# Performance work log

Measured on AMD Instinct MI355X. Metric: run time of the kernel, lower is better.

The kernel has to match this reference:

```python
import jax, jax.numpy as jnp
import numpy as np

T, N, F_IN, H1, H2, F_OUT = 48, 4096, 64, 64, 32, 64

def setup_inputs() -> dict:
    key = jax.random.key(0)
    ks = jax.random.split(key, 14)
    sc = 0.05
    x = jax.random.normal(ks[0], (T, N, F_IN), jnp.float32)
    adj = jax.random.uniform(ks[1], (N, N), jnp.float32) / N  # roughly row-normalized dense adjacency
    fc_w = jax.random.normal(ks[2], (F_IN, H1), jnp.float32) * sc
    fc_b = jnp.zeros((H1,), jnp.float32)
    Wz = jax.random.normal(ks[3], (H1, F_OUT), jnp.float32) * sc
    Wr = jax.random.normal(ks[4], (H1, F_OUT), jnp.float32) * sc
    Wh = jax.random.normal(ks[5], (H1, F_OUT), jnp.float32) * sc
    Lz = jax.random.normal(ks[6], (2 * F_OUT, F_OUT), jnp.float32) * sc
    Lr = jax.random.normal(ks[7], (2 * F_OUT, F_OUT), jnp.float32) * sc
    Lh = jax.random.normal(ks[8], (2 * F_OUT, F_OUT), jnp.float32) * sc
    bz = jnp.zeros((F_OUT,), jnp.float32)
    br = jnp.zeros((F_OUT,), jnp.float32)
    bh = jnp.zeros((F_OUT,), jnp.float32)
    return {"x": x, "adj": adj, "fc_w": fc_w, "fc_b": fc_b,
            "Wz": Wz, "Wr": Wr, "Wh": Wh,
            "Lz": Lz, "Lr": Lr, "Lh": Lh,
            "bz": bz, "br": br, "bh": bh}

def reference(x, adj, fc_w, fc_b, Wz, Wr, Wh, Lz, Lr, Lh, bz, br, bh):
    # relu(fc(x)) followed by relu(unsqueeze) == single relu
    xh = jax.nn.relu(x @ fc_w + fc_b)          # [T, N, H1]
    h0 = jnp.zeros((N, F_OUT), x.dtype)

    def step(h, xi):
        # TGCN cell: dense graph conv A @ (X W) feeding GRU-style gates
        az = adj @ (xi @ Wz)                   # [N, F_OUT]
        ar = adj @ (xi @ Wr)
        ah = adj @ (xi @ Wh)
        z = jax.nn.sigmoid(jnp.concatenate([az, h], axis=-1) @ Lz + bz)
        r = jax.nn.sigmoid(jnp.concatenate([ar, h], axis=-1) @ Lr + br)
        h_tilde = jnp.tanh(jnp.concatenate([ah, h * r], axis=-1) @ Lh + bh)
        h_new = z * h + (1.0 - z) * h_tilde
        return h_new, None

    h, _ = jax.lax.scan(step, h0, xh)
    return h[None]                              # [1, N, F_OUT]
```

## Files before the change

### kernel.cpp

```cpp
#include <hip/hip_runtime.h>

typedef unsigned short u16;
typedef unsigned char u8;
typedef short s16x8 __attribute__((ext_vector_type(8)));
typedef unsigned short u16x4 __attribute__((ext_vector_type(4)));
typedef float f32x4 __attribute__((ext_vector_type(4)));
typedef int i32x4 __attribute__((ext_vector_type(4)));
typedef int i32x8 __attribute__((ext_vector_type(8)));

#define AS1 __attribute__((address_space(1)))
#define AS3 __attribute__((address_space(3)))

__device__ __forceinline__ void g2l16(const void* g, void* l) {
  __builtin_amdgcn_global_load_lds((const AS1 void*)g, (AS3 void*)l, 16, 0, 0);
}

__device__ __forceinline__ float b2f(u16 u) {
  union { unsigned int i; float f; } x; x.i = ((unsigned int)u) << 16; return x.f;
}
__device__ __forceinline__ u16 f2b(float f) {
  unsigned int u = __builtin_bit_cast(unsigned int, f);
  return (u16)((u + 0x7fffu + ((u >> 16) & 1u)) >> 16);
}
__device__ __forceinline__ u8 f2e4m3(float v) {
  int p = __builtin_amdgcn_cvt_pk_fp8_f32(v, 0.f, 0, false);
  return (u8)(p & 0xff);
}
__device__ __forceinline__ float sigm(float x) { return 1.f / (1.f + __expf(-x)); }
__device__ __forceinline__ float tanh_f(float x) { return 2.f / (1.f + __expf(-2.f * x)) - 1.f; }


__global__ __launch_bounds__(256) void kpre(
    const float* __restrict__ a, u8* __restrict__ ab,
    const float* __restrict__ fcw, const float* __restrict__ fcb,
    const float* __restrict__ x, u8* __restrict__ xht,
    const float* __restrict__ Wz, const float* __restrict__ Wr, const float* __restrict__ Wh,
    const float* __restrict__ Lz, const float* __restrict__ Lr, const float* __restrict__ Lh,
    u16* __restrict__ wct, u16* __restrict__ lbt) {
  int b = blockIdx.x, tid = threadIdx.x;
  if (b < 4096) {
    size_t idx = (size_t)b * 256 + tid;
    const float4* src = (const float4*)a;
    unsigned int* dst = (unsigned int*)ab;
#pragma unroll
    for (int k = 0; k < 4; ++k) {
      float4 v = src[idx + (size_t)k * 1048576];
      unsigned int p = __builtin_amdgcn_cvt_pk_fp8_f32(v.x * 4096.f, v.y * 4096.f, 0, false);
      p = __builtin_amdgcn_cvt_pk_fp8_f32(v.z * 4096.f, v.w * 4096.f, p, true);
      dst[idx + (size_t)k * 1048576] = p;
    }
    return;
  }
  if (b < 4144) {
    int idx = (b - 4096) * 256 + tid;
    int c_cat = idx >> 6, hh = idx & 63;
    int g = c_cat >> 6, c = c_cat & 63;
    const float* W = (g == 0) ? Wz : (g == 1) ? Wr : Wh;
    const float* L = (g == 0) ? Lz : (g == 1) ? Lr : Lh;
    float acc = 0.f;
    for (int m = 0; m < 64; ++m) acc += W[hh * 64 + m] * L[m * 64 + c];
    wct[c_cat * 64 + hh] = f2b(acc);
    return;
  }
  if (b < 4147) {
    int g = b - 4144;
    const float* L = (g == 0) ? Lz : (g == 1) ? Lr : Lh;
    for (int i = 0; i < 16; ++i) {
      int idx = tid * 16 + i; int c = idx >> 6, hh = idx & 63;
      lbt[g * 4096 + c * 64 + hh] = f2b(L[(64 + hh) * 64 + c]);
    }
    return;
  }
  int kb = b - 4147;
  int t = kb >> 5, n0 = (kb & 31) * 128;
  __shared__ __align__(16) u16 xs[128 * 72];
  __shared__ __align__(16) u16 fw[64 * 72];
  __shared__ __align__(16) u8 xh8[64 * 128];
  __shared__ float fb[64];
  int w = tid >> 6, l = tid & 63;
#pragma unroll
  for (int i = 0; i < 16; ++i) {
    int idx = tid + i * 256;
    int h = idx & 63, f = idx >> 6;
    fw[h * 72 + f] = f2b(fcw[f * 64 + h]);
  }
  const float4* xg = (const float4*)(x + ((size_t)t * 4096 + n0) * 64);
#pragma unroll
  for (int i = 0; i < 8; ++i) {
    int f = tid + i * 256;
    float4 v = xg[f];
    u16x4 p; p[0] = f2b(v.x); p[1] = f2b(v.y); p[2] = f2b(v.z); p[3] = f2b(v.w);
    *(u16x4*)&xs[(f >> 4) * 72 + (f & 15) * 4] = p;
  }
  if (tid < 64) fb[tid] = fcb[tid];
  __syncthreads();

  int lm = l & 15, q = l >> 4;
  f32x4 acc[4][2];
#pragma unroll
  for (int i = 0; i < 4; ++i)
#pragma unroll
    for (int j = 0; j < 2; ++j)
#pragma unroll
      for (int r = 0; r < 4; ++r) acc[i][j][r] = 0.f;
#pragma unroll
  for (int s = 0; s < 2; ++s) {
    s16x8 af[4], bf[2];
#pragma unroll
    for (int i = 0; i < 4; ++i) af[i] = *(const s16x8*)&fw[(16 * i + lm) * 72 + 32 * s + q * 8];
#pragma unroll
    for (int j = 0; j < 2; ++j) bf[j] = *(const s16x8*)&xs[(32 * w + 16 * j + lm) * 72 + 32 * s + q * 8];
#pragma unroll
    for (int i = 0; i < 4; ++i)
#pragma unroll
      for (int j = 0; j < 2; ++j)
        acc[i][j] = __builtin_amdgcn_mfma_f32_16x16x32_bf16(af[i], bf[j], acc[i][j], 0, 0, 0);
  }
#pragma unroll
  for (int i = 0; i < 4; ++i)
#pragma unroll
    for (int j = 0; j < 2; ++j) {
      int node = 32 * w + 16 * j + lm;
      int h0 = 16 * i + q * 4;
#pragma unroll
      for (int r = 0; r < 4; ++r) {
        float v = acc[i][j][r] + fb[h0 + r];
        xh8[(h0 + r) * 128 + node] = f2e4m3(v > 0.f ? v : 0.f);
      }
    }
  __syncthreads();
  {
    int h = tid >> 2, seg = tid & 3;
    u8* dst = xht + (size_t)(t * 64 + h) * 4096 + n0 + seg * 32;
    const u8* src = &xh8[h * 128 + seg * 32];
    *(i32x4*)dst = *(const i32x4*)src;
    *(i32x4*)(dst + 16) = *(const i32x4*)(src + 16);
  }
}

__global__ __launch_bounds__(256) void k2(
    const u8* __restrict__ A, const u8* __restrict__ B, u16* __restrict__ M) {
  __shared__ __align__(16) u8 sh[81920];
  int tid = threadIdx.x, w = tid >> 6, l = tid & 63;
  int nt = blockIdx.x, mt = blockIdx.y;
  const u8* Ab = A + (size_t)mt * 128 * 4096;
  const u8* Bb = B + (size_t)nt * 192 * 4096;
  int lm = l & 15, q = l >> 4;
  int wm = w >> 1, wn = w & 1;
  int srow = l >> 3, scol = l & 7;
  f32x4 acc[4][6];
#pragma unroll
  for (int i = 0; i < 4; ++i)
#pragma unroll
    for (int j = 0; j < 6; ++j)
#pragma unroll
      for (int r = 0; r < 4; ++r) acc[i][j][r] = 0.f;

#define STAGE(bsel, kk)                                                       \
  do {                                                                        \
    u8* As_ = sh + (bsel) * 40960;                                            \
    u8* Bs_ = As_ + 16384;                                                    \
    _Pragma("unroll") for (int j = 0; j < 4; ++j) {      \
      int r0 = 32 * w + 8 * j;                                                \
      int row = r0 + srow;                                                    \
      int c = (scol - row) & 7;                                               \
      g2l16(Ab + (size_t)row * 4096 + (kk) + c * 16, As_ + r0 * 128);         \
    }                                                                         \
    _Pragma("unroll") for (int j = 0; j < 6; ++j) {      \
      int r0 = 48 * w + 8 * j;                                                \
      int row = r0 + srow;                                                    \
      int c = (scol - row) & 7;                                               \
      g2l16(Bb + (size_t)row * 4096 + (kk) + c * 16, Bs_ + r0 * 128);         \
    }                                                                         \
  } while (0)

  STAGE(0, 0);
  __syncthreads();

  for (int it = 0; it < 32; ++it) {
    int k0b = it * 128;
    int cur = it & 1;
    if (it < 31) STAGE(cur ^ 1, k0b + 128);
    const u8* As = sh + cur * 40960;
    const u8* Bs = As + 16384;
    i32x8 a8[4];
#pragma unroll
    for (int i = 0; i < 4; ++i) {
      int ra = 64 * wm + 16 * i + lm;
      int p0 = (2 * q + ra) & 7, p1 = (2 * q + 1 + ra) & 7;
      i32x4 lo = *(const i32x4*)&As[ra * 128 + p0 * 16];
      i32x4 hi = *(const i32x4*)&As[ra * 128 + p1 * 16];
      a8[i] = __builtin_shufflevector(lo, hi, 0, 1, 2, 3, 4, 5, 6, 7);
    }
#pragma unroll
    for (int j = 0; j < 6; ++j) {
      int rb = 96 * wn + 16 * j + lm;
      int q0 = (2 * q + rb) & 7, q1 = (2 * q + 1 + rb) & 7;
      i32x4 lo2 = *(const i32x4*)&Bs[rb * 128 + q0 * 16];
      i32x4 hi2 = *(const i32x4*)&Bs[rb * 128 + q1 * 16];
      i32x8 b8 = __builtin_shufflevector(lo2, hi2, 0, 1, 2, 3, 4, 5, 6, 7);
#pragma unroll
      for (int i = 0; i < 4; ++i)
        acc[i][j] = __builtin_amdgcn_mfma_scale_f32_16x16x128_f8f6f4(
            a8[i], b8, acc[i][j], 0, 0, 0, 127, 0, 127);
    }
    __syncthreads();
  }
#undef STAGE

  u16* tb = (u16*)sh;
  const float sc = 1.f / 4096.f;
#pragma unroll
  for (int p = 0; p < 2; ++p) {
    if (p) __syncthreads();
    if (wm == p) {
#pragma unroll
      for (int i = 0; i < 4; ++i)
#pragma unroll
        for (int j = 0; j < 6; ++j)
#pragma unroll
          for (int r = 0; r < 4; ++r)
            tb[(16 * i + 4 * q + r) * 200 + 96 * wn + 16 * j + lm] = f2b(acc[i][j][r] * sc);
    }
    __syncthreads();
    int row = tid >> 2, seg = tid & 3;
    u16* dst = M + (size_t)(mt * 128 + p * 64 + row) * 3072 + nt * 192 + seg * 48;
    const u16* src = &tb[row * 200 + seg * 48];
#pragma unroll
    for (int v = 0; v < 6; ++v)
      *(i32x4*)(dst + 8 * v) = *(const i32x4*)(src + 8 * v);
  }
}

__global__ __launch_bounds__(256) void k3(
    const u16* __restrict__ M, const u16* __restrict__ wct, const u16* __restrict__ lbt,
    const float* __restrict__ bz, const float* __restrict__ br, const float* __restrict__ bh,
    float* __restrict__ out) {
  __shared__ __align__(16) u16 hhi[16 * 72], hlo[16 * 72];
  __shared__ __align__(16) u16 rhi[16 * 72], rlo[16 * 72];
  int tid = threadIdx.x, w = tid >> 6, l = tid & 63;
  int nb0 = blockIdx.x * 16;
  int lm = l & 15, q = l >> 4;
  int cb = 16 * w + q * 4;
  s16x8 afw[3][2], afl[3][2];
#pragma unroll
  for (int g = 0; g < 3; ++g)
#pragma unroll
    for (int s = 0; s < 2; ++s) {
      afw[g][s] = *(const s16x8*)&wct[(size_t)(g * 64 + 16 * w + lm) * 64 + 32 * s + q * 8];
      afl[g][s] = *(const s16x8*)&lbt[(size_t)(g * 64 + 16 * w + lm) * 64 + 32 * s + q * 8];
    }
  for (int i = tid; i < 16 * 72; i += 256) { hhi[i] = 0; hlo[i] = 0; }
  f32x4 bzv, brv, bhv, hv;
#pragma unroll
  for (int r = 0; r < 4; ++r) {
    bzv[r] = bz[cb + r]; brv[r] = br[cb + r]; bhv[r] = bh[cb + r]; hv[r] = 0.f;
  }
  __syncthreads();

  const u16* Mrow = M + (size_t)(nb0 + lm) * 3072;
  s16x8 Mn[2];
  Mn[0] = *(const s16x8*)&Mrow[q * 8];
  Mn[1] = *(const s16x8*)&Mrow[32 + q * 8];

  for (int t = 0; t < 48; ++t) {
    s16x8 Mc[2] = {Mn[0], Mn[1]};
    if (t < 47) {
      Mn[0] = *(const s16x8*)&Mrow[(t + 1) * 64 + q * 8];
      Mn[1] = *(const s16x8*)&Mrow[(t + 1) * 64 + 32 + q * 8];
    }
    f32x4 uzw, uzh, urw, urh;
#pragma unroll
    for (int r = 0; r < 4; ++r) { uzw[r] = 0.f; uzh[r] = 0.f; urw[r] = 0.f; urh[r] = 0.f; }
#pragma unroll
    for (int s = 0; s < 2; ++s) {
      s16x8 hh = *(const s16x8*)&hhi[lm * 72 + 32 * s + q * 8];
      s16x8 hl = *(const s16x8*)&hlo[lm * 72 + 32 * s + q * 8];
      uzw = __builtin_amdgcn_mfma_f32_16x16x32_bf16(afw[0][s], Mc[s], uzw, 0, 0, 0);
      uzh = __builtin_amdgcn_mfma_f32_16x16x32_bf16(afl[0][s], hh, uzh, 0, 0, 0);
      uzh = __builtin_amdgcn_mfma_f32_16x16x32_bf16(afl[0][s], hl, uzh, 0, 0, 0);
      urw = __builtin_amdgcn_mfma_f32_16x16x32_bf16(afw[1][s], Mc[s], urw, 0, 0, 0);
      urh = __builtin_amdgcn_mfma_f32_16x16x32_bf16(afl[1][s], hh, urh, 0, 0, 0);
      urh = __builtin_amdgcn_mfma_f32_16x16x32_bf16(afl[1][s], hl, urh, 0, 0, 0);
    }
    f32x4 zv, rv;
#pragma unroll
    for (int r = 0; r < 4; ++r) {
      zv[r] = sigm(uzw[r] + uzh[r] + bzv[r]);
      rv[r] = sigm(urw[r] + urh[r] + brv[r]);
    }
    {
      u16x4 phi, plo;
#pragma unroll
      for (int r = 0; r < 4; ++r) {
        float p = hv[r] * rv[r];
        u16 hi = f2b(p); phi[r] = hi; plo[r] = f2b(p - b2f(hi));
      }
      *(u16x4*)&rhi[lm * 72 + cb] = phi;
      *(u16x4*)&rlo[lm * 72 + cb] = plo;
    }
    __syncthreads();
    f32x4 uhw, uhh;
#pragma unroll
    for (int r = 0; r < 4; ++r) { uhw[r] = 0.f; uhh[r] = 0.f; }
#pragma unroll
    for (int s = 0; s < 2; ++s) {
      s16x8 rh = *(const s16x8*)&rhi[lm * 72 + 32 * s + q * 8];
      s16x8 rl = *(const s16x8*)&rlo[lm * 72 + 32 * s + q * 8];
      uhw = __builtin_amdgcn_mfma_f32_16x16x32_bf16(afw[2][s], Mc[s], uhw, 0, 0, 0);
      uhh = __builtin_amdgcn_mfma_f32_16x16x32_bf16(afl[2][s], rh, uhh, 0, 0, 0);
      uhh = __builtin_amdgcn_mfma_f32_16x16x32_bf16(afl[2][s], rl, uhh, 0, 0, 0);
    }
    {
      u16x4 phi, plo;
#pragma unroll
      for (int r = 0; r < 4; ++r) {
        float th = tanh_f(uhw[r] + uhh[r] + bhv[r]);
        float hn = zv[r] * hv[r] + (1.f - zv[r]) * th;
        hv[r] = hn;
        u16 hi = f2b(hn); phi[r] = hi; plo[r] = f2b(hn - b2f(hi));
      }
      *(u16x4*)&hhi[lm * 72 + cb] = phi;
      *(u16x4*)&hlo[lm * 72 + cb] = plo;
    }
    __syncthreads();
  }
#pragma unroll
  for (int r = 0; r < 4; ++r)
    out[(size_t)(nb0 + lm) * 64 + cb + r] = hv[r];
}

extern "C" void kernel_launch(void* const* d_in, const int* in_sizes, int n_in,
                              void* d_out, int out_size, void* d_ws, size_t ws_size,
                              hipStream_t stream) {
  const float* x   = (const float*)d_in[0];
  const float* adj = (const float*)d_in[1];
  const float* fcw = (const float*)d_in[2];
  const float* fcb = (const float*)d_in[3];
  const float* Wz  = (const float*)d_in[4];
  const float* Wr  = (const float*)d_in[5];
  const float* Wh  = (const float*)d_in[6];
  const float* Lz  = (const float*)d_in[7];
  const float* Lr  = (const float*)d_in[8];
  const float* Lh  = (const float*)d_in[9];
  const float* bz  = (const float*)d_in[10];
  const float* br  = (const float*)d_in[11];
  const float* bh  = (const float*)d_in[12];
  char* ws = (char*)d_ws;
  u8*  xht  = (u8*)(ws);
  u8*  adj8 = (u8*)(ws + (size_t)12582912);
  u16* Mm   = (u16*)(ws + (size_t)29360128);
  u16* wct  = (u16*)(ws + (size_t)54525952);
  u16* lbt  = (u16*)(ws + (size_t)54550528);
  float* outp = (float*)d_out;

  hipLaunchKernelGGL(kpre, dim3(5683), dim3(256), 0, stream,
                     adj, adj8, fcw, fcb, x, xht, Wz, Wr, Wh, Lz, Lr, Lh, wct, lbt);
  hipLaunchKernelGGL(k2, dim3(16, 32), dim3(256), 0, stream, adj8, xht, Mm);
  hipLaunchKernelGGL(k3, dim3(256), dim3(256), 0, stream, Mm, wct, lbt, bz, br, bh, outp);
}
```

Measured before the change: 259.3 us.

## Precompute next-step input MFMAs off the critical path and swizzle LDS hidden state

In the recurrent GRU kernel, the input-side MFMAs (M times gate weights, seeded with the bias) for step t+1 are now issued before the end-of-step barrier, so only the hidden-state MFMAs remain on the serial dependency chain. The hi and lo hidden-state products are split into independent accumulators to shorten MFMA dependency chains. The LDS layout changes from padded 72-element rows to 64-element rows with an XOR swizzle, meant to avoid bank conflicts while using less shared memory. It adds live registers for the precomputed accumulators.

```diff
diff --git a/kernel.cpp b/kernel.cpp
--- a/kernel.cpp
+++ b/kernel.cpp
@@ -236,12 +236,16 @@
     const u16* __restrict__ M, const u16* __restrict__ wct, const u16* __restrict__ lbt,
     const float* __restrict__ bz, const float* __restrict__ br, const float* __restrict__ bh,
     float* __restrict__ out) {
-  __shared__ __align__(16) u16 hhi[16 * 72], hlo[16 * 72];
-  __shared__ __align__(16) u16 rhi[16 * 72], rlo[16 * 72];
+  __shared__ __align__(16) u16 hhi[1024], hlo[1024];
+  __shared__ __align__(16) u16 rhi[1024], rlo[1024];
   int tid = threadIdx.x, w = tid >> 6, l = tid & 63;
   int nb0 = blockIdx.x * 16;
   int lm = l & 15, q = l >> 4;
+  int am = lm & 7;
   int cb = 16 * w + q * 4;
+  int rd0 = lm * 64 + ((q ^ am) * 8);
+  int rd1 = lm * 64 + (((4 + q) ^ am) * 8);
+  int wi  = lm * 64 + (((2 * w + (q >> 1)) ^ am) * 8) + 4 * (q & 1);
   s16x8 afw[3][2], afl[3][2];
 #pragma unroll
   for (int g = 0; g < 3; ++g)
@@ -250,44 +254,46 @@
       afw[g][s] = *(const s16x8*)&wct[(size_t)(g * 64 + 16 * w + lm) * 64 + 32 * s + q * 8];
       afl[g][s] = *(const s16x8*)&lbt[(size_t)(g * 64 + 16 * w + lm) * 64 + 32 * s + q * 8];
     }
-  for (int i = tid; i < 16 * 72; i += 256) { hhi[i] = 0; hlo[i] = 0; }
+  for (int i = tid; i < 1024; i += 256) { hhi[i] = 0; hlo[i] = 0; }
   f32x4 bzv, brv, bhv, hv;
 #pragma unroll
   for (int r = 0; r < 4; ++r) {
     bzv[r] = bz[cb + r]; brv[r] = br[cb + r]; bhv[r] = bh[cb + r]; hv[r] = 0.f;
   }
+  const f32x4 zf = {0.f, 0.f, 0.f, 0.f};
   __syncthreads();
 
   const u16* Mrow = M + (size_t)(nb0 + lm) * 3072;
   s16x8 Mn[2];
   Mn[0] = *(const s16x8*)&Mrow[q * 8];
   Mn[1] = *(const s16x8*)&Mrow[32 + q * 8];
+  f32x4 uzwC = __builtin_amdgcn_mfma_f32_16x16x32_bf16(afw[0][0], Mn[0], bzv, 0, 0, 0);
+  uzwC = __builtin_amdgcn_mfma_f32_16x16x32_bf16(afw[0][1], Mn[1], uzwC, 0, 0, 0);
+  f32x4 urwC = __builtin_amdgcn_mfma_f32_16x16x32_bf16(afw[1][0], Mn[0], brv, 0, 0, 0);
+  urwC = __builtin_amdgcn_mfma_f32_16x16x32_bf16(afw[1][1], Mn[1], urwC, 0, 0, 0);
+  f32x4 uhwC = __builtin_amdgcn_mfma_f32_16x16x32_bf16(afw[2][0], Mn[0], bhv, 0, 0, 0);
+  uhwC = __builtin_amdgcn_mfma_f32_16x16x32_bf16(afw[2][1], Mn[1], uhwC, 0, 0, 0);
 
   for (int t = 0; t < 48; ++t) {
-    s16x8 Mc[2] = {Mn[0], Mn[1]};
     if (t < 47) {
       Mn[0] = *(const s16x8*)&Mrow[(t + 1) * 64 + q * 8];
       Mn[1] = *(const s16x8*)&Mrow[(t + 1) * 64 + 32 + q * 8];
     }
-    f32x4 uzw, uzh, urw, urh;
-#pragma unroll
-    for (int r = 0; r < 4; ++r) { uzw[r] = 0.f; uzh[r] = 0.f; urw[r] = 0.f; urh[r] = 0.f; }
-#pragma unroll
-    for (int s = 0; s < 2; ++s) {
-      s16x8 hh = *(const s16x8*)&hhi[lm * 72 + 32 * s + q * 8];
-      s16x8 hl = *(const s16x8*)&hlo[lm * 72 + 32 * s + q * 8];
-      uzw = __builtin_amdgcn_mfma_f32_16x16x32_bf16(afw[0][s], Mc[s], uzw, 0, 0, 0);
-      uzh = __builtin_amdgcn_mfma_f32_16x16x32_bf16(afl[0][s], hh, uzh, 0, 0, 0);
-      uzh = __builtin_amdgcn_mfma_f32_16x16x32_bf16(afl[0][s], hl, uzh, 0, 0, 0);
-      urw = __builtin_amdgcn_mfma_f32_16x16x32_bf16(afw[1][s], Mc[s], urw, 0, 0, 0);
-      urh = __builtin_amdgcn_mfma_f32_16x16x32_bf16(afl[1][s], hh, urh, 0, 0, 0);
-      urh = __builtin_amdgcn_mfma_f32_16x16x32_bf16(afl[1][s], hl, urh, 0, 0, 0);
-    }
+    s16x8 hh0 = *(const s16x8*)&hhi[rd0], hh1 = *(const s16x8*)&hhi[rd1];
+    s16x8 hl0 = *(const s16x8*)&hlo[rd0], hl1 = *(const s16x8*)&hlo[rd1];
+    f32x4 uzA = __builtin_amdgcn_mfma_f32_16x16x32_bf16(afl[0][0], hh0, uzwC, 0, 0, 0);
+    uzA = __builtin_amdgcn_mfma_f32_16x16x32_bf16(afl[0][1], hh1, uzA, 0, 0, 0);
+    f32x4 uzB = __builtin_amdgcn_mfma_f32_16x16x32_bf16(afl[0][0], hl0, zf, 0, 0, 0);
+    uzB = __builtin_amdgcn_mfma_f32_16x16x32_bf16(afl[0][1], hl1, uzB, 0, 0, 0);
+    f32x4 urA = __builtin_amdgcn_mfma_f32_16x16x32_bf16(afl[1][0], hh0, urwC, 0, 0, 0);
+    urA = __builtin_amdgcn_mfma_f32_16x16x32_bf16(afl[1][1], hh1, urA, 0, 0, 0);
+    f32x4 urB = __builtin_amdgcn_mfma_f32_16x16x32_bf16(afl[1][0], hl0, zf, 0, 0, 0);
+    urB = __builtin_amdgcn_mfma_f32_16x16x32_bf16(afl[1][1], hl1, urB, 0, 0, 0);
     f32x4 zv, rv;
 #pragma unroll
     for (int r = 0; r < 4; ++r) {
-      zv[r] = sigm(uzw[r] + uzh[r] + bzv[r]);
-      rv[r] = sigm(urw[r] + urh[r] + brv[r]);
+      zv[r] = sigm(uzA[r] + uzB[r]);
+      rv[r] = sigm(urA[r] + urB[r]);
     }
     {
       u16x4 phi, plo;
@@ -296,32 +302,35 @@
         float p = hv[r] * rv[r];
         u16 hi = f2b(p); phi[r] = hi; plo[r] = f2b(p - b2f(hi));
       }
-      *(u16x4*)&rhi[lm * 72 + cb] = phi;
-      *(u16x4*)&rlo[lm * 72 + cb] = plo;
+      *(u16x4*)&rhi[wi] = phi;
+      *(u16x4*)&rlo[wi] = plo;
     }
     __syncthreads();
-    f32x4 uhw, uhh;
-#pragma unroll
-    for (int r = 0; r < 4; ++r) { uhw[r] = 0.f; uhh[r] = 0.f; }
-#pragma unroll
-    for (int s = 0; s < 2; ++s) {
-      s16x8 rh = *(const s16x8*)&rhi[lm * 72 + 32 * s + q * 8];
-      s16x8 rl = *(const s16x8*)&rlo[lm * 72 + 32 * s + q * 8];
-      uhw = __builtin_amdgcn_mfma_f32_16x16x32_bf16(afw[2][s], Mc[s], uhw, 0, 0, 0);
-      uhh = __builtin_amdgcn_mfma_f32_16x16x32_bf16(afl[2][s], rh, uhh, 0, 0, 0);
-      uhh = __builtin_amdgcn_mfma_f32_16x16x32_bf16(afl[2][s], rl, uhh, 0, 0, 0);
-    }
+    s16x8 rh0 = *(const s16x8*)&rhi[rd0], rh1 = *(const s16x8*)&rhi[rd1];
+    s16x8 rl0 = *(const s16x8*)&rlo[rd0], rl1 = *(const s16x8*)&rlo[rd1];
+    f32x4 uhA = __builtin_amdgcn_mfma_f32_16x16x32_bf16(afl[2][0], rh0, uhwC, 0, 0, 0);
+    uhA = __builtin_amdgcn_mfma_f32_16x16x32_bf16(afl[2][1], rh1, uhA, 0, 0, 0);
+    f32x4 uhB = __builtin_amdgcn_mfma_f32_16x16x32_bf16(afl[2][0], rl0, zf, 0, 0, 0);
+    uhB = __builtin_amdgcn_mfma_f32_16x16x32_bf16(afl[2][1], rl1, uhB, 0, 0, 0);
     {
       u16x4 phi, plo;
 #pragma unroll
       for (int r = 0; r < 4; ++r) {
-        float th = tanh_f(uhw[r] + uhh[r] + bhv[r]);
+        float th = tanh_f(uhA[r] + uhB[r]);
         float hn = zv[r] * hv[r] + (1.f - zv[r]) * th;
         hv[r] = hn;
         u16 hi = f2b(hn); phi[r] = hi; plo[r] = f2b(hn - b2f(hi));
       }
-      *(u16x4*)&hhi[lm * 72 + cb] = phi;
-      *(u16x4*)&hlo[lm * 72 + cb] = plo;
+      *(u16x4*)&hhi[wi] = phi;
+      *(u16x4*)&hlo[wi] = plo;
+    }
+    if (t < 47) {
+      uzwC = __builtin_amdgcn_mfma_f32_16x16x32_bf16(afw[0][0], Mn[0], bzv, 0, 0, 0);
+      uzwC = __builtin_amdgcn_mfma_f32_16x16x32_bf16(afw[0][1], Mn[1], uzwC, 0, 0, 0);
+      urwC = __builtin_amdgcn_mfma_f32_16x16x32_bf16(afw[1][0], Mn[0], brv, 0, 0, 0);
+      urwC = __builtin_amdgcn_mfma_f32_16x16x32_bf16(afw[1][1], Mn[1], urwC, 0, 0, 0);
+      uhwC = __builtin_amdgcn_mfma_f32_16x16x32_bf16(afw[2][0], Mn[0], bhv, 0, 0, 0);
+      uhwC = __builtin_amdgcn_mfma_f32_16x16x32_bf16(afw[2][1], Mn[1], uhwC, 0, 0, 0);
     }
     __syncthreads();
   }
```

After: 256.4 us. No clear change (-1.1%).

## Restructure recurrent kernel to single-wave blocks without barriers and precompute input projections

Applied to the files above, without the earlier changes.

The GRU recurrence kernel moves from four waves per block, each owning 16 output columns, to one 64-thread wave per block that computes all 64 output columns for its 16 nodes. This removes both __syncthreads per timestep, since LDS h/r exchange is now intra-wave. The input-projection MFMAs (M·W) for the next step are issued ahead, with the bias folded into the accumulator. W is staged in LDS while the L weights stay in registers. Each wave now carries four times the MFMA work serially, and occupancy is one wave per block over 256 blocks, so latency hiding depends on ILP within the wave.

```diff
diff --git a/kernel.cpp b/kernel.cpp
--- a/kernel.cpp
+++ b/kernel.cpp
@@ -232,102 +232,139 @@
   }
 }
 
-__global__ __launch_bounds__(256) void k3(
+__global__ __launch_bounds__(64, 1) void k3(
     const u16* __restrict__ M, const u16* __restrict__ wct, const u16* __restrict__ lbt,
     const float* __restrict__ bz, const float* __restrict__ br, const float* __restrict__ bh,
     float* __restrict__ out) {
+  __shared__ __align__(16) u16 wlds[192 * 72];
   __shared__ __align__(16) u16 hhi[16 * 72], hlo[16 * 72];
   __shared__ __align__(16) u16 rhi[16 * 72], rlo[16 * 72];
-  int tid = threadIdx.x, w = tid >> 6, l = tid & 63;
-  int nb0 = blockIdx.x * 16;
+  int l = threadIdx.x & 63;
+  int nw0 = blockIdx.x * 16;
   int lm = l & 15, q = l >> 4;
-  int cb = 16 * w + q * 4;
-  s16x8 afw[3][2], afl[3][2];
+
+  for (int idx = l; idx < 1536; idx += 64) {
+    int row = idx >> 3, cs = idx & 7;
+    *(s16x8*)&wlds[row * 72 + cs * 8] = *(const s16x8*)&wct[row * 64 + cs * 8];
+  }
+  for (int i = l; i < 1152; i += 64) { hhi[i] = 0; hlo[i] = 0; }
+
+  s16x8 afl[3][4][2];
 #pragma unroll
   for (int g = 0; g < 3; ++g)
 #pragma unroll
-    for (int s = 0; s < 2; ++s) {
-      afw[g][s] = *(const s16x8*)&wct[(size_t)(g * 64 + 16 * w + lm) * 64 + 32 * s + q * 8];
-      afl[g][s] = *(const s16x8*)&lbt[(size_t)(g * 64 + 16 * w + lm) * 64 + 32 * s + q * 8];
-    }
-  for (int i = tid; i < 16 * 72; i += 256) { hhi[i] = 0; hlo[i] = 0; }
-  f32x4 bzv, brv, bhv, hv;
-#pragma unroll
-  for (int r = 0; r < 4; ++r) {
-    bzv[r] = bz[cb + r]; brv[r] = br[cb + r]; bhv[r] = bh[cb + r]; hv[r] = 0.f;
-  }
-  __syncthreads();
-
-  const u16* Mrow = M + (size_t)(nb0 + lm) * 3072;
+    for (int f = 0; f < 4; ++f)
+#pragma unroll
+      for (int s = 0; s < 2; ++s)
+        afl[g][f][s] = *(const s16x8*)&lbt[g * 4096 + (16 * f + lm) * 64 + 32 * s + 8 * q];
+
+  f32x4 bzv[4], brv[4], bhv[4], hv[4];
+#pragma unroll
+  for (int f = 0; f < 4; ++f)
+#pragma unroll
+    for (int r = 0; r < 4; ++r) {
+      bzv[f][r] = bz[16 * f + 4 * q + r];
+      brv[f][r] = br[16 * f + 4 * q + r];
+      bhv[f][r] = bh[16 * f + 4 * q + r];
+      hv[f][r] = 0.f;
+    }
+  const f32x4 zf = {0.f, 0.f, 0.f, 0.f};
+
+  const u16* Mrow = M + (size_t)(nw0 + lm) * 3072;
   s16x8 Mn[2];
-  Mn[0] = *(const s16x8*)&Mrow[q * 8];
-  Mn[1] = *(const s16x8*)&Mrow[32 + q * 8];
+  Mn[0] = *(const s16x8*)&Mrow[8 * q];
+  Mn[1] = *(const s16x8*)&Mrow[32 + 8 * q];
+
+#define MPART(uC, g, bias)                                                    \
+  _Pragma("unroll") for (int f = 0; f < 4; ++f) {                             \
+    s16x8 w0 = *(const s16x8*)&wlds[((g) * 64 + 16 * f + lm) * 72 + 8 * q];   \
+    s16x8 w1 = *(const s16x8*)&wlds[((g) * 64 + 16 * f + lm) * 72 + 32 + 8 * q]; \
+    uC[f] = __builtin_amdgcn_mfma_f32_16x16x32_bf16(w0, Mn[0], bias[f], 0, 0, 0); \
+    uC[f] = __builtin_amdgcn_mfma_f32_16x16x32_bf16(w1, Mn[1], uC[f], 0, 0, 0); \
+  }
+
+  f32x4 uzwC[4], urwC[4], uhwC[4];
+  MPART(uzwC, 0, bzv)
+  MPART(urwC, 1, brv)
+  MPART(uhwC, 2, bhv)
 
   for (int t = 0; t < 48; ++t) {
-    s16x8 Mc[2] = {Mn[0], Mn[1]};
     if (t < 47) {
-      Mn[0] = *(const s16x8*)&Mrow[(t + 1) * 64 + q * 8];
-      Mn[1] = *(const s16x8*)&Mrow[(t + 1) * 64 + 32 + q * 8];
-    }
-    f32x4 uzw, uzh, urw, urh;
-#pragma unroll
-    for (int r = 0; r < 4; ++r) { uzw[r] = 0.f; uzh[r] = 0.f; urw[r] = 0.f; urh[r] = 0.f; }
-#pragma unroll
-    for (int s = 0; s < 2; ++s) {
-      s16x8 hh = *(const s16x8*)&hhi[lm * 72 + 32 * s + q * 8];
-      s16x8 hl = *(const s16x8*)&hlo[lm * 72 + 32 * s + q * 8];
-      uzw = __builtin_amdgcn_mfma_f32_16x16x32_bf16(afw[0][s], Mc[s], uzw, 0, 0, 0);
-      uzh = __builtin_amdgcn_mfma_f32_16x16x32_bf16(afl[0][s], hh, uzh, 0, 0, 0);
-      uzh = __builtin_amdgcn_mfma_f32_16x16x32_bf16(afl[0][s], hl, uzh, 0, 0, 0);
-      urw = __builtin_amdgcn_mfma_f32_16x16x32_bf16(afw[1][s], Mc[s], urw, 0, 0, 0);
-      urh = __builtin_amdgcn_mfma_f32_16x16x32_bf16(afl[1][s], hh, urh, 0, 0, 0);
-      urh = __builtin_amdgcn_mfma_f32_16x16x32_bf16(afl[1][s], hl, urh, 0, 0, 0);
-    }
-    f32x4 zv, rv;
-#pragma unroll
-    for (int r = 0; r < 4; ++r) {
-      zv[r] = sigm(uzw[r] + uzh[r] + bzv[r]);
-      rv[r] = sigm(urw[r] + urh[r] + brv[r]);
-    }
-    {
+      Mn[0] = *(const s16x8*)&Mrow[(t + 1) * 64 + 8 * q];
+      Mn[1] = *(const s16x8*)&Mrow[(t + 1) * 64 + 32 + 8 * q];
+    }
+    s16x8 hh0 = *(const s16x8*)&hhi[lm * 72 + 8 * q];
+    s16x8 hh1 = *(const s16x8*)&hhi[lm * 72 + 32 + 8 * q];
+    s16x8 hl0 = *(const s16x8*)&hlo[lm * 72 + 8 * q];
+    s16x8 hl1 = *(const s16x8*)&hlo[lm * 72 + 32 + 8 * q];
+    f32x4 zA[4], zB[4], rA[4], rB[4];
+#pragma unroll
+    for (int f = 0; f < 4; ++f) {
+      zA[f] = __builtin_amdgcn_mfma_f32_16x16x32_bf16(afl[0][f][0], hh0, uzwC[f], 0, 0, 0);
+      zA[f] = __builtin_amdgcn_mfma_f32_16x16x32_bf16(afl[0][f][1], hh1, zA[f], 0, 0, 0);
+      zB[f] = __builtin_amdgcn_mfma_f32_16x16x32_bf16(afl[0][f][0], hl0, zf, 0, 0, 0);
+      zB[f] = __builtin_amdgcn_mfma_f32_16x16x32_bf16(afl[0][f][1], hl1, zB[f], 0, 0, 0);
+      rA[f] = __builtin_amdgcn_mfma_f32_16x16x32_bf16(afl[1][f][0], hh0, urwC[f], 0, 0, 0);
+      rA[f] = __builtin_amdgcn_mfma_f32_16x16x32_bf16(afl[1][f][1], hh1, rA[f], 0, 0, 0);
+      rB[f] = __builtin_amdgcn_mfma_f32_16x16x32_bf16(afl[1][f][0], hl0, zf, 0, 0, 0);
+      rB[f] = __builtin_amdgcn_mfma_f32_16x16x32_bf16(afl[1][f][1], hl1, rB[f], 0, 0, 0);
+    }
+    f32x4 zv[4], rv[4];
+#pragma unroll
+    for (int f = 0; f < 4; ++f)
+#pragma unroll
+      for (int r = 0; r < 4; ++r) {
+        zv[f][r] = sigm(zA[f][r] + zB[f][r]);
+        rv[f][r] = sigm(rA[f][r] + rB[f][r]);
+      }
+#pragma unroll
+    for (int f = 0; f < 4; ++f) {
       u16x4 phi, plo;
 #pragma unroll
       for (int r = 0; r < 4; ++r) {
-        float p = hv[r] * rv[r];
+        float p = hv[f][r] * rv[f][r];
         u16 hi = f2b(p); phi[r] = hi; plo[r] = f2b(p - b2f(hi));
       }
-      *(u16x4*)&rhi[lm * 72 + cb] = phi;
-      *(u16x4*)&rlo[lm * 72 + cb] = plo;
-    }
-    __syncthreads();
-    f32x4 uhw, uhh;
-#pragma unroll
-    for (int r = 0; r < 4; ++r) { uhw[r] = 0.f; uhh[r] = 0.f; }
-#pragma unroll
-    for (int s = 0; s < 2; ++s) {
-      s16x8 rh = *(const s16x8*)&rhi[lm * 72 + 32 * s + q * 8];
-      s16x8 rl = *(const s16x8*)&rlo[lm * 72 + 32 * s + q * 8];
-      uhw = __builtin_amdgcn_mfma_f32_16x16x32_bf16(afw[2][s], Mc[s], uhw, 0, 0, 0);
-      uhh = __builtin_amdgcn_mfma_f32_16x16x32_bf16(afl[2][s], rh, uhh, 0, 0, 0);
-      uhh = __builtin_amdgcn_mfma_f32_16x16x32_bf16(afl[2][s], rl, uhh, 0, 0, 0);
-    }
-    {
+      *(u16x4*)&rhi[lm * 72 + 16 * f + 4 * q] = phi;
+      *(u16x4*)&rlo[lm * 72 + 16 * f + 4 * q] = plo;
+    }
+    s16x8 rh0 = *(const s16x8*)&rhi[lm * 72 + 8 * q];
+    s16x8 rh1 = *(const s16x8*)&rhi[lm * 72 + 32 + 8 * q];
+    s16x8 rl0 = *(const s16x8*)&rlo[lm * 72 + 8 * q];
+    s16x8 rl1 = *(const s16x8*)&rlo[lm * 72 + 32 + 8 * q];
+    f32x4 hA[4], hB[4];
+#pragma unroll
+    for (int f = 0; f < 4; ++f) {
+      hA[f] = __builtin_amdgcn_mfma_f32_16x16x32_bf16(afl[2][f][0], rh0, uhwC[f], 0, 0, 0);
+      hA[f] = __builtin_amdgcn_mfma_f32_16x16x32_bf16(afl[2][f][1], rh1, hA[f], 0, 0, 0);
+      hB[f] = __builtin_amdgcn_mfma_f32_16x16x32_bf16(afl[2][f][0], rl0, zf, 0, 0, 0);
+      hB[f] = __builtin_amdgcn_mfma_f32_16x16x32_bf16(afl[2][f][1], rl1, hB[f], 0, 0, 0);
+    }
+#pragma unroll
+    for (int f = 0; f < 4; ++f) {
       u16x4 phi, plo;
 #pragma unroll
       for (int r = 0; r < 4; ++r) {
-        float th = tanh_f(uhw[r] + uhh[r] + bhv[r]);
-        float hn = zv[r] * hv[r] + (1.f - zv[r]) * th;
-        hv[r] = hn;
+        float th = tanh_f(hA[f][r] + hB[f][r]);
+        float hn = zv[f][r] * hv[f][r] + (1.f - zv[f][r]) * th;
+        hv[f][r] = hn;
         u16 hi = f2b(hn); phi[r] = hi; plo[r] = f2b(hn - b2f(hi));
       }
-      *(u16x4*)&hhi[lm * 72 + cb] = phi;
-      *(u16x4*)&hlo[lm * 72 + cb] = plo;
-    }
-    __syncthreads();
-  }
-#pragma unroll
-  for (int r = 0; r < 4; ++r)
-    out[(size_t)(nb0 + lm) * 64 + cb + r] = hv[r];
+      *(u16x4*)&hhi[lm * 72 + 16 * f + 4 * q] = phi;
+      *(u16x4*)&hlo[lm * 72 + 16 * f + 4 * q] = plo;
+    }
+    if (t < 47) {
+      MPART(uzwC, 0, bzv)
+      MPART(urwC, 1, brv)
+      MPART(uhwC, 2, bhv)
+    }
+  }
+#undef MPART
+#pragma unroll
+  for (int f = 0; f < 4; ++f)
+#pragma unroll
+    for (int r = 0; r < 4; ++r)
+      out[(size_t)(nw0 + lm) * 64 + 16 * f + 4 * q + r] = hv[f][r];
 }
 
 extern "C" void kernel_launch(void* const* d_in, const int* in_sizes, int n_in,
@@ -357,5 +394,5 @@
   hipLaunchKernelGGL(kpre, dim3(5683), dim3(256), 0, stream,
                      adj, adj8, fcw, fcb, x, xht, Wz, Wr, Wh, Lz, Lr, Lh, wct, lbt);
   hipLaunchKernelGGL(k2, dim3(16, 32), dim3(256), 0, stream, adj8, xht, Mm);
-  hipLaunchKernelGGL(k3, dim3(256), dim3(256), 0, stream, Mm, wct, lbt, bz, br, bh, outp);
-}
+  hipLaunchKernelGGL(k3, dim3(256), dim3(64), 0, stream, Mm, wct, lbt, bz, br, bh, outp);
+}
```

After: 353.7 us. 36.4% more time.
